# Optimization experiments

Hardware: AMD Instinct MI355X
Metric: run time of the kernel (lower is better)

Reference implementation:

```python
import jax, jax.numpy as jnp
import numpy as np

B = 8192
IN = 2048
H = 2048


def setup_inputs() -> dict:
    key = jax.random.key(0)
    ks = jax.random.split(key, 11)
    s_w = 1.0 / np.sqrt(IN + H)  # torch Linear default init scale
    inp = {
        "input": jax.random.normal(ks[0], (B, IN), jnp.float32),
        "h_prev": jax.random.normal(ks[1], (B, H), jnp.float32),
        "c_prev": jax.random.normal(ks[2], (B, H), jnp.float32),
        "Wf": jax.random.normal(ks[3], (H, IN + H), jnp.float32) * s_w,
        "bf": jax.random.normal(ks[4], (H,), jnp.float32) * s_w,
        "Wi": jax.random.normal(ks[5], (H, IN + H), jnp.float32) * s_w,
        "bi": jax.random.normal(ks[6], (H,), jnp.float32) * s_w,
        "Wg": jax.random.normal(ks[7], (H, IN + H), jnp.float32) * s_w,
        "bg": jax.random.normal(ks[8], (H,), jnp.float32) * s_w,
        "Wo": jax.random.normal(ks[9], (H, IN + H), jnp.float32) * s_w,
        "bo": jax.random.normal(ks[10], (H,), jnp.float32) * s_w,
    }
    return inp


def reference(input, h_prev, c_prev, Wf, bf, Wi, bi, Wg, bg, Wo, bo):
    # combined: [B, IN+H]
    combined = jnp.concatenate([input, h_prev], axis=1)
    # Fuse the 4 gate GEMMs into one: W_all [4H, IN+H]
    W_all = jnp.concatenate([Wf, Wi, Wg, Wo], axis=0)
    b_all = jnp.concatenate([bf, bi, bg, bo], axis=0)
    gates = combined @ W_all.T + b_all  # [B, 4H]
    f_, i_, g_, o_ = jnp.split(gates, 4, axis=1)
    f = jax.nn.sigmoid(f_)
    i = jax.nn.sigmoid(i_)
    g = jnp.tanh(g_)
    o = jax.nn.sigmoid(o_)
    c = f * c_prev + i * g
    h = o * jnp.tanh(c)
    return (h, c)
```

## Files before the change

### kernel.cpp

```cpp
#include <hip/hip_runtime.h>
#include <stdint.h>


#define BQ 8192
#define INF 2048
#define HH 2048
#define KK 4096

typedef __attribute__((ext_vector_type(8))) short short8;
typedef __attribute__((ext_vector_type(8))) unsigned short ushort8;
typedef __attribute__((ext_vector_type(4))) float floatx4;

__device__ __forceinline__ unsigned short f2b(float f) {
    unsigned u = __float_as_uint(f);
    u += 0x7fff + ((u >> 16) & 1);
    return (unsigned short)(u >> 16);
}
__device__ __forceinline__ ushort8 cvt8(float4 a, float4 b) {
    ushort8 y;
    y[0] = f2b(a.x); y[1] = f2b(a.y); y[2] = f2b(a.z); y[3] = f2b(a.w);
    y[4] = f2b(b.x); y[5] = f2b(b.y); y[6] = f2b(b.z); y[7] = f2b(b.w);
    return y;
}
__device__ __forceinline__ float fsig(float x) {
    return 1.f / (1.f + __expf(-x));
}
__device__ __forceinline__ float ftanh(float x) {
    return 1.f - 2.f / (__expf(2.f * x) + 1.f);
}

__global__ __launch_bounds__(256) void pack_all(
    const float4* __restrict__ inp, const float4* __restrict__ hp,
    const float4* __restrict__ w0, const float4* __restrict__ w1,
    const float4* __restrict__ w2, const float4* __restrict__ w3,
    unsigned short* __restrict__ comb, unsigned short* __restrict__ wpk)
{
    const int NC16 = BQ * INF / 16;
    int v = blockIdx.x * 256 + threadIdx.x;
    if (v < 2 * NC16) {
        int isH = v >= NC16;
        int u16 = v - (isH ? NC16 : 0);
        const float4* src = isH ? hp : inp;
        float4 x0 = src[u16 * 4];
        float4 x1 = src[u16 * 4 + 1];
        float4 x2 = src[u16 * 4 + 2];
        float4 x3 = src[u16 * 4 + 3];
        int u = u16 * 16;
        int b = u >> 11;
        int k = u & 2047;
        unsigned short* d = comb + (size_t)b * KK + k + (isH ? INF : 0);
        *(ushort8*)d       = cvt8(x0, x1);
        *(ushort8*)(d + 8) = cvt8(x2, x3);
    } else {
        int w = v - 2 * NC16;
        size_t e = (size_t)w * 16;
        int g = (int)(e >> 23);
        int u = (int)(e & ((1u << 23) - 1));
        int h = u >> 12;
        int k = u & 4095;
        const float4* src = (g == 0) ? w0 : (g == 1) ? w1 : (g == 2) ? w2 : w3;
        float4 x0 = src[(u >> 2)];
        float4 x1 = src[(u >> 2) + 1];
        float4 x2 = src[(u >> 2) + 2];
        float4 x3 = src[(u >> 2) + 3];
        int p = ((h >> 5) << 7) + (g << 5) + (h & 31);
        unsigned short* d = wpk + (size_t)p * KK + k;
        *(ushort8*)d       = cvt8(x0, x1);
        *(ushort8*)(d + 8) = cvt8(x2, x3);
    }
}

__global__ __launch_bounds__(512, 2) void lstm_fused(
    const unsigned short* __restrict__ A,
    const unsigned short* __restrict__ W,
    const float* __restrict__ cprev,
    const float* __restrict__ bf_, const float* __restrict__ bi_,
    const float* __restrict__ bg_, const float* __restrict__ bo_,
    float* __restrict__ out)
{
    __shared__ unsigned short lds[65536];
    char* ldsb = (char*)lds;

    const int t    = threadIdx.x;
    const int wv   = t >> 6;
    const int lane = t & 63;
    const int wm   = wv >> 1;
    const int wn   = wv & 1;
    const int fr   = lane & 15;
    const int fq   = lane >> 4;

    int lin = blockIdx.y * 32 + blockIdx.x;
    lin = (lin & 7) * 128 + (lin >> 3);
    const int m0 = (lin >> 5) << 8;
    const int n0 = (lin & 31) << 8;

    const int koff = ((lane & 7) ^ (lane >> 3)) << 3;
    const unsigned short* aR = A + (size_t)(m0 + wv * 16 + (lane >> 3)) * KK + koff;
    const unsigned short* bR = W + (size_t)(n0 + wv * 16 + (lane >> 3)) * KK + koff;
    const int stgOff = wv * 16 * 128;

    const int x7    = fr & 7;
    const int aBase = (wm >> 1) * 16384 + ((wm & 1) * 64 + fr) * 128;
    const int bBase = 32768 + wn * 16384 + fr * 128;

    floatx4 acc[4][8];
#pragma unroll
    for (int i = 0; i < 4; ++i)
#pragma unroll
        for (int j = 0; j < 8; ++j) acc[i][j] = (floatx4)0.f;

    short8 aA[2][2];
    short8 bb[8][2];

#define STAGE(srcbase, ldsoff, kk)                                              \
    do {                                                                        \
        __builtin_amdgcn_global_load_lds(                                       \
            (const __attribute__((address_space(1))) void*)((srcbase) + (kk)),  \
            (__attribute__((address_space(3))) void*)(ldsb + (ldsoff) + stgOff),\
            16, 0, 0);                                                          \
        __builtin_amdgcn_global_load_lds(                                       \
            (const __attribute__((address_space(1))) void*)((srcbase) + 8 * KK + (kk)), \
            (__attribute__((address_space(3))) void*)(ldsb + (ldsoff) + stgOff + 1024), \
            16, 0, 0);                                                          \
    } while (0)

    auto LDA = [&](int side, int i, short8* d) {
        const char* p = ldsb + side * 65536 + aBase + i * 2048;
        d[0] = *(const short8*)(p + ((fq ^ x7) << 4));
        d[1] = *(const short8*)(p + (((4 + fq) ^ x7) << 4));
    };
    auto LDB = [&](int side, int j, short8* d) {
        const char* p = ldsb + side * 65536 + bBase + j * 2048;
        d[0] = *(const short8*)(p + ((fq ^ x7) << 4));
        d[1] = *(const short8*)(p + (((4 + fq) ^ x7) << 4));
    };
    auto MM = [&](const short8* a, const short8* b, floatx4& c) {
        c = __builtin_amdgcn_mfma_f32_16x16x32_bf16(a[0], b[0], c, 0, 0, 0);
        c = __builtin_amdgcn_mfma_f32_16x16x32_bf16(a[1], b[1], c, 0, 0, 0);
    };

#define BAR()  __builtin_amdgcn_s_barrier()
#define SB0()  __builtin_amdgcn_sched_barrier(0)
#define VM4()  do { asm volatile("s_waitcnt vmcnt(4)" ::: "memory"); SB0(); } while (0)

    STAGE(aR, 0, 0);
    STAGE(aR + 128 * KK, 16384, 0);
    STAGE(bR, 32768, 0);
    STAGE(bR + 128 * KK, 49152, 0);
    STAGE(bR, 98304, 64);
    STAGE(bR + 128 * KK, 114688, 64);
    VM4();
    BAR();

#pragma unroll 1
    for (int it = 0; it < 32; ++it) {
        const int k1 = ((2 * it + 1) & 63) << 6;
        const int k2 = ((2 * it + 2) & 63) << 6;
        const int k3 = ((2 * it + 3) & 63) << 6;

        LDA(0, 0, aA[0]); LDA(0, 1, aA[1]);
        LDB(0, 0, bb[0]); LDB(0, 1, bb[1]); LDB(0, 2, bb[2]); LDB(0, 3, bb[3]);
        STAGE(aR, 65536, k1);
        SB0(); BAR();
        __builtin_amdgcn_s_setprio(1);
#pragma unroll
        for (int ia = 0; ia < 2; ++ia)
#pragma unroll
            for (int j = 0; j < 4; ++j) MM(aA[ia], bb[j], acc[ia][j]);
        __builtin_amdgcn_s_setprio(0);
        BAR();

        LDB(0, 4, bb[4]); LDB(0, 5, bb[5]); LDB(0, 6, bb[6]); LDB(0, 7, bb[7]);
        STAGE(aR + 128 * KK, 81920, k1);
        SB0(); BAR();
        __builtin_amdgcn_s_setprio(1);
#pragma unroll
        for (int ia = 0; ia < 2; ++ia)
#pragma unroll
            for (int j = 0; j < 4; ++j) MM(aA[ia], bb[4 + j], acc[ia][4 + j]);
        __builtin_amdgcn_s_setprio(0);
        BAR();

        LDA(0, 2, aA[0]); LDA(0, 3, aA[1]);
        STAGE(bR, 32768, k2);
        SB0(); BAR();
        __builtin_amdgcn_s_setprio(1);
#pragma unroll
        for (int ia = 0; ia < 2; ++ia)
#pragma unroll
            for (int j = 0; j < 4; ++j) MM(aA[ia], bb[4 + j], acc[2 + ia][4 + j]);
        __builtin_amdgcn_s_setprio(0);
        BAR();

        STAGE(bR + 128 * KK, 49152, k2);
        SB0(); BAR();
        __builtin_amdgcn_s_setprio(1);
#pragma unroll
        for (int ia = 0; ia < 2; ++ia)
#pragma unroll
            for (int j = 0; j < 4; ++j) MM(aA[ia], bb[j], acc[2 + ia][j]);
        __builtin_amdgcn_s_setprio(0);
        VM4();
        BAR();

        LDA(1, 0, aA[0]); LDA(1, 1, aA[1]);
        LDB(1, 0, bb[0]); LDB(1, 1, bb[1]); LDB(1, 2, bb[2]); LDB(1, 3, bb[3]);
        STAGE(aR, 0, k2);
        SB0(); BAR();
        __builtin_amdgcn_s_setprio(1);
#pragma unroll
        for (int ia = 0; ia < 2; ++ia)
#pragma unroll
            for (int j = 0; j < 4; ++j) MM(aA[ia], bb[j], acc[ia][j]);
        __builtin_amdgcn_s_setprio(0);
        BAR();

        LDB(1, 4, bb[4]); LDB(1, 5, bb[5]); LDB(1, 6, bb[6]); LDB(1, 7, bb[7]);
        STAGE(aR + 128 * KK, 16384, k2);
        SB0(); BAR();
        __builtin_amdgcn_s_setprio(1);
#pragma unroll
        for (int ia = 0; ia < 2; ++ia)
#pragma unroll
            for (int j = 0; j < 4; ++j) MM(aA[ia], bb[4 + j], acc[ia][4 + j]);
        __builtin_amdgcn_s_setprio(0);
        BAR();

        LDA(1, 2, aA[0]); LDA(1, 3, aA[1]);
        STAGE(bR, 98304, k3);
        SB0(); BAR();
        __builtin_amdgcn_s_setprio(1);
#pragma unroll
        for (int ia = 0; ia < 2; ++ia)
#pragma unroll
            for (int j = 0; j < 4; ++j) MM(aA[ia], bb[4 + j], acc[2 + ia][4 + j]);
        __builtin_amdgcn_s_setprio(0);
        BAR();

        STAGE(bR + 128 * KK, 114688, k3);
        SB0(); BAR();
        __builtin_amdgcn_s_setprio(1);
#pragma unroll
        for (int ia = 0; ia < 2; ++ia)
#pragma unroll
            for (int j = 0; j < 4; ++j) MM(aA[ia], bb[j], acc[2 + ia][j]);
        __builtin_amdgcn_s_setprio(0);
        VM4();
        BAR();
    }

    const int hb = (n0 >> 2) + wn * 32;
    float bF[2], bI[2], bG[2], bO[2];
#pragma unroll
    for (int jh = 0; jh < 2; ++jh) {
        int h = hb + jh * 16 + fr;
        bF[jh] = bf_[h]; bI[jh] = bi_[h]; bG[jh] = bg_[h]; bO[jh] = bo_[h];
    }
    const int rowb = m0 + wm * 64 + fq * 4;
#pragma unroll
    for (int i = 0; i < 4; ++i) {
#pragma unroll
        for (int r = 0; r < 4; ++r) {
            int row = rowb + i * 16 + r;
#pragma unroll
            for (int jh = 0; jh < 2; ++jh) {
                int h = hb + jh * 16 + fr;
                size_t gi = (size_t)row * HH + h;
                float xf = acc[i][0 + jh][r] + bF[jh];
                float xi = acc[i][2 + jh][r] + bI[jh];
                float xg = acc[i][4 + jh][r] + bG[jh];
                float xo = acc[i][6 + jh][r] + bO[jh];
                float f  = fsig(xf);
                float ii = fsig(xi);
                float g  = ftanh(xg);
                float o  = fsig(xo);
                float c  = f * cprev[gi] + ii * g;
                float hv = o * ftanh(c);
                out[gi] = hv;
                out[(size_t)BQ * HH + gi] = c;
            }
        }
    }
}

extern "C" void kernel_launch(void* const* d_in, const int* in_sizes, int n_in,
                              void* d_out, int out_size, void* d_ws, size_t ws_size,
                              hipStream_t stream) {
    const float* input  = (const float*)d_in[0];
    const float* h_prev = (const float*)d_in[1];
    const float* c_prev = (const float*)d_in[2];
    const float* Wf = (const float*)d_in[3];
    const float* bf_ = (const float*)d_in[4];
    const float* Wi = (const float*)d_in[5];
    const float* bi_ = (const float*)d_in[6];
    const float* Wg = (const float*)d_in[7];
    const float* bg_ = (const float*)d_in[8];
    const float* Wo = (const float*)d_in[9];
    const float* bo_ = (const float*)d_in[10];
    float* out = (float*)d_out;

    unsigned short* combined = (unsigned short*)d_ws;
    unsigned short* Wpk = (unsigned short*)d_ws + (size_t)BQ * KK;

    pack_all<<<dim3(16384), 256, 0, stream>>>(
        (const float4*)input, (const float4*)h_prev,
        (const float4*)Wf, (const float4*)Wi, (const float4*)Wg, (const float4*)Wo,
        combined, Wpk);
    lstm_fused<<<dim3(32, 32), 512, 0, stream>>>(
        combined, Wpk, c_prev, bf_, bi_, bg_, bo_, out);
}
```

Baseline: 818.2 us.

## Hold all A fragments in registers and stream B fragments per cluster

Restructures the inner K loop so each wave keeps all four A sub-tiles resident and loads only two B sub-tiles per MFMA cluster, instead of keeping eight B sub-tiles and two A sub-tiles. The global-to-LDS staging order is changed so A is prefetched one step ahead of B. This cuts fragment register pressure (12 vs 20 short8 pairs) and spreads LDS reads more evenly across the four clusters. In exchange the prefetch dependency ordering changes, which risks stalls if the staged B data is not ready by the time it is read.

New measurement: 806.6 us. No clear change (-1.4%).

```diff
diff --git a/kernel.cpp b/kernel.cpp
--- a/kernel.cpp
+++ b/kernel.cpp
@@ -109,8 +109,8 @@
 #pragma unroll
         for (int j = 0; j < 8; ++j) acc[i][j] = (floatx4)0.f;
 
-    short8 aA[2][2];
-    short8 bb[8][2];
+    short8 aA[4][2];
+    short8 bb[2][2];
 
 #define STAGE(srcbase, ldsoff, kk)                                              \
     do {                                                                        \
@@ -143,12 +143,23 @@
 #define SB0()  __builtin_amdgcn_sched_barrier(0)
 #define VM4()  do { asm volatile("s_waitcnt vmcnt(4)" ::: "memory"); SB0(); } while (0)
 
+#define CLUSTER(p)                                                    \
+    do {                                                              \
+        __builtin_amdgcn_s_setprio(1);                                \
+        _Pragma("unroll")                                             \
+        for (int i = 0; i < 4; ++i) {                                 \
+            MM(aA[i], bb[0], acc[i][2 * (p)]);                        \
+            MM(aA[i], bb[1], acc[i][2 * (p) + 1]);                    \
+        }                                                             \
+        __builtin_amdgcn_s_setprio(0);                                \
+    } while (0)
+
     STAGE(aR, 0, 0);
     STAGE(aR + 128 * KK, 16384, 0);
     STAGE(bR, 32768, 0);
     STAGE(bR + 128 * KK, 49152, 0);
-    STAGE(bR, 98304, 64);
-    STAGE(bR + 128 * KK, 114688, 64);
+    STAGE(aR, 65536, 64);
+    STAGE(aR + 128 * KK, 81920, 64);
     VM4();
     BAR();
 
@@ -158,93 +169,55 @@
         const int k2 = ((2 * it + 2) & 63) << 6;
         const int k3 = ((2 * it + 3) & 63) << 6;
 
-        LDA(0, 0, aA[0]); LDA(0, 1, aA[1]);
-        LDB(0, 0, bb[0]); LDB(0, 1, bb[1]); LDB(0, 2, bb[2]); LDB(0, 3, bb[3]);
-        STAGE(aR, 65536, k1);
-        SB0(); BAR();
-        __builtin_amdgcn_s_setprio(1);
-#pragma unroll
-        for (int ia = 0; ia < 2; ++ia)
-#pragma unroll
-            for (int j = 0; j < 4; ++j) MM(aA[ia], bb[j], acc[ia][j]);
-        __builtin_amdgcn_s_setprio(0);
-        BAR();
-
-        LDB(0, 4, bb[4]); LDB(0, 5, bb[5]); LDB(0, 6, bb[6]); LDB(0, 7, bb[7]);
-        STAGE(aR + 128 * KK, 81920, k1);
-        SB0(); BAR();
-        __builtin_amdgcn_s_setprio(1);
-#pragma unroll
-        for (int ia = 0; ia < 2; ++ia)
-#pragma unroll
-            for (int j = 0; j < 4; ++j) MM(aA[ia], bb[4 + j], acc[ia][4 + j]);
-        __builtin_amdgcn_s_setprio(0);
-        BAR();
-
-        LDA(0, 2, aA[0]); LDA(0, 3, aA[1]);
+        LDA(0, 0, aA[0]); LDB(0, 0, bb[0]); LDB(0, 1, bb[1]);
+        LDA(0, 1, aA[1]); LDA(0, 2, aA[2]); LDA(0, 3, aA[3]);
+        STAGE(bR, 98304, k1);
+        SB0(); BAR();
+        CLUSTER(0);
+        BAR();
+
+        LDB(0, 2, bb[0]); LDB(0, 3, bb[1]);
+        STAGE(bR + 128 * KK, 114688, k1);
+        SB0(); BAR();
+        CLUSTER(1);
+        BAR();
+
+        LDB(0, 4, bb[0]); LDB(0, 5, bb[1]);
+        STAGE(aR, 0, k2);
+        SB0(); BAR();
+        CLUSTER(2);
+        BAR();
+
+        LDB(0, 6, bb[0]); LDB(0, 7, bb[1]);
+        STAGE(aR + 128 * KK, 16384, k2);
+        SB0(); BAR();
+        CLUSTER(3);
+        VM4();
+        BAR();
+
+        LDA(1, 0, aA[0]); LDB(1, 0, bb[0]); LDB(1, 1, bb[1]);
+        LDA(1, 1, aA[1]); LDA(1, 2, aA[2]); LDA(1, 3, aA[3]);
         STAGE(bR, 32768, k2);
         SB0(); BAR();
-        __builtin_amdgcn_s_setprio(1);
-#pragma unroll
-        for (int ia = 0; ia < 2; ++ia)
-#pragma unroll
-            for (int j = 0; j < 4; ++j) MM(aA[ia], bb[4 + j], acc[2 + ia][4 + j]);
-        __builtin_amdgcn_s_setprio(0);
-        BAR();
-
+        CLUSTER(0);
+        BAR();
+
+        LDB(1, 2, bb[0]); LDB(1, 3, bb[1]);
         STAGE(bR + 128 * KK, 49152, k2);
         SB0(); BAR();
-        __builtin_amdgcn_s_setprio(1);
-#pragma unroll
-        for (int ia = 0; ia < 2; ++ia)
-#pragma unroll
-            for (int j = 0; j < 4; ++j) MM(aA[ia], bb[j], acc[2 + ia][j]);
-        __builtin_amdgcn_s_setprio(0);
-        VM4();
-        BAR();
-
-        LDA(1, 0, aA[0]); LDA(1, 1, aA[1]);
-        LDB(1, 0, bb[0]); LDB(1, 1, bb[1]); LDB(1, 2, bb[2]); LDB(1, 3, bb[3]);
-        STAGE(aR, 0, k2);
-        SB0(); BAR();
-        __builtin_amdgcn_s_setprio(1);
-#pragma unroll
-        for (int ia = 0; ia < 2; ++ia)
-#pragma unroll
-            for (int j = 0; j < 4; ++j) MM(aA[ia], bb[j], acc[ia][j]);
-        __builtin_amdgcn_s_setprio(0);
-        BAR();
-
-        LDB(1, 4, bb[4]); LDB(1, 5, bb[5]); LDB(1, 6, bb[6]); LDB(1, 7, bb[7]);
-        STAGE(aR + 128 * KK, 16384, k2);
-        SB0(); BAR();
-        __builtin_amdgcn_s_setprio(1);
-#pragma unroll
-        for (int ia = 0; ia < 2; ++ia)
-#pragma unroll
-            for (int j = 0; j < 4; ++j) MM(aA[ia], bb[4 + j], acc[ia][4 + j]);
-        __builtin_amdgcn_s_setprio(0);
-        BAR();
-
-        LDA(1, 2, aA[0]); LDA(1, 3, aA[1]);
-        STAGE(bR, 98304, k3);
-        SB0(); BAR();
-        __builtin_amdgcn_s_setprio(1);
-#pragma unroll
-        for (int ia = 0; ia < 2; ++ia)
-#pragma unroll
-            for (int j = 0; j < 4; ++j) MM(aA[ia], bb[4 + j], acc[2 + ia][4 + j]);
-        __builtin_amdgcn_s_setprio(0);
-        BAR();
-
-        STAGE(bR + 128 * KK, 114688, k3);
-        SB0(); BAR();
-        __builtin_amdgcn_s_setprio(1);
-#pragma unroll
-        for (int ia = 0; ia < 2; ++ia)
-#pragma unroll
-            for (int j = 0; j < 4; ++j) MM(aA[ia], bb[j], acc[2 + ia][j]);
-        __builtin_amdgcn_s_setprio(0);
+        CLUSTER(1);
+        BAR();
+
+        LDB(1, 4, bb[0]); LDB(1, 5, bb[1]);
+        STAGE(aR, 65536, k3);
+        SB0(); BAR();
+        CLUSTER(2);
+        BAR();
+
+        LDB(1, 6, bb[0]); LDB(1, 7, bb[1]);
+        STAGE(aR + 128 * KK, 81920, k3);
+        SB0(); BAR();
+        CLUSTER(3);
         VM4();
         BAR();
     }
```
